# Performance work log

Measured on AMD Instinct MI355X. Metric: run time of the kernel, lower is better.

The kernel has to match this reference:

```python
import jax, jax.numpy as jnp
import numpy as np

B, L, H, NH, DH, FF, NL, REL = 2, 1024, 256, 8, 32, 1024, 2, 100
SCALE = np.sqrt(DH).astype(np.float32)
EPS = 1e-5


def _ln(x, g, b):
    m = jnp.mean(x, axis=-1, keepdims=True)
    v = jnp.mean(jnp.square(x - m), axis=-1, keepdims=True)
    return (x - m) * jax.lax.rsqrt(v + EPS) * g + b


def setup_inputs() -> dict:
    key = jax.random.key(0)
    ks = jax.random.split(key, 20)
    s = 0.02
    Ek = jax.random.normal(ks[0], (REL, DH), jnp.float32) * s
    Ev = jax.random.normal(ks[1], (REL, DH), jnp.float32) * s
    Ek = Ek.at[0].set(0.0)  # padding_idx=0
    Ev = Ev.at[0].set(0.0)
    return {
        "inputs": jax.random.normal(ks[2], (B, L, H), jnp.float32),
        "Wq": jax.random.normal(ks[3], (NL, H, H), jnp.float32) * s,
        "Wk": jax.random.normal(ks[4], (NL, H, H), jnp.float32) * s,
        "Wv": jax.random.normal(ks[5], (NL, H, H), jnp.float32) * s,
        "Wo": jax.random.normal(ks[6], (NL, H, H), jnp.float32) * s,
        "bo": jnp.zeros((NL, H), jnp.float32),
        "W1": jax.random.normal(ks[7], (NL, H, FF), jnp.float32) * s,
        "b1": jnp.zeros((NL, FF), jnp.float32),
        "W2": jax.random.normal(ks[8], (NL, FF, H), jnp.float32) * s,
        "b2": jnp.zeros((NL, H), jnp.float32),
        "ln1_g": jnp.ones((NL, H), jnp.float32),
        "ln1_b": jnp.zeros((NL, H), jnp.float32),
        "ln2_g": jnp.ones((NL, H), jnp.float32),
        "ln2_b": jnp.zeros((NL, H), jnp.float32),
        "Ek": Ek,
        "Ev": Ev,
        "relations": jax.random.randint(ks[9], (B, L, L), 0, REL, jnp.int32),
        "relations_mask": jax.random.randint(ks[10], (B, L, L), 0, 2, jnp.int32).astype(bool),
    }


def reference(inputs, Wq, Wk, Wv, Wo, bo, W1, b1, W2, b2,
              ln1_g, ln1_b, ln2_g, ln2_b, Ek, Ev, relations, relations_mask):
    # relation embeddings shared across layers and heads: (B,L,L,DH)
    rel_k = Ek[relations]
    rel_v = Ev[relations]
    neg = relations_mask.astype(jnp.float32) * (-1e20)  # (B,L,L)
    x = inputs
    for l in range(NL):
        q = (x @ Wq[l]).reshape(B, L, NH, DH)
        k = (x @ Wk[l]).reshape(B, L, NH, DH)
        v = (x @ Wv[l]).reshape(B, L, NH, DH)
        # scores: q.(k_j + rel_k[i,j]) decomposed to avoid (B,H,L,L,DH)
        e = (jnp.einsum('bihd,bjhd->bhij', q, k)
             + jnp.einsum('bihd,bijd->bhij', q, rel_k)) / SCALE
        e = e + neg[:, None, :, :]
        a = jax.nn.softmax(e, axis=-1)  # (B,NH,L,L)
        o = (jnp.einsum('bhij,bjhd->bihd', a, v)
             + jnp.einsum('bhij,bijd->bihd', a, rel_v)).reshape(B, L, H)
        o = o @ Wo[l] + bo[l]
        x = _ln(x + o, ln1_g[l], ln1_b[l])
        ff = jax.nn.relu(x @ W1[l] + b1[l]) @ W2[l] + b2[l]
        x = _ln(x + ff, ln2_g[l], ln2_b[l])
    return x
```

## Files before the change

kernel.cpp:

```cpp
#include <hip/hip_runtime.h>


typedef unsigned short ushortt;
typedef __attribute__((ext_vector_type(8))) short short8;
typedef __attribute__((ext_vector_type(4))) float f32x4;

__device__ __forceinline__ ushortt f2bf(float f) {
  union { float f; unsigned int u; } c; c.f = f;
  unsigned int r = c.u + 0x7fffu + ((c.u >> 16) & 1u);
  return (ushortt)(r >> 16);
}
__device__ __forceinline__ unsigned int pk2(float a, float b) {
  return (unsigned int)f2bf(a) | ((unsigned int)f2bf(b) << 16);
}

__global__ void wcvt_all_k(const float* __restrict__ Wq, const float* __restrict__ Wk,
                           const float* __restrict__ Wv, const float* __restrict__ Wo,
                           const float* __restrict__ W1, const float* __restrict__ W2,
                           ushortt* __restrict__ wbuf) {
  int i = blockIdx.x * blockDim.x + threadIdx.x;
  int st = gridDim.x * blockDim.x;
  for (; i < 1572864; i += st) {
    int l = (i >= 786432) ? 1 : 0;
    int e = i - (l ? 786432 : 0);
    size_t o_w = (size_t)l * 65536, o_w1 = (size_t)l * 262144;
    float v;
    if (e < 262144) {
      int which = e >> 16;
      int loc = e & 65535;
      int k = loc & 255, n = loc >> 8;
      const float* W = (which == 0) ? Wq : (which == 1) ? Wk : (which == 2) ? Wv : Wo;
      v = W[o_w + ((size_t)k << 8) + n];
    } else if (e < 524288) {
      int loc = e - 262144;
      int k = loc & 255, n = loc >> 8;
      v = W1[o_w1 + ((size_t)k << 10) + n];
    } else {
      int loc = e - 524288;
      int k = loc & 1023, n = loc >> 10;
      v = W2[o_w1 + ((size_t)k << 8) + n];
    }
    wbuf[i] = f2bf(v);
  }
}

__global__ __launch_bounds__(256) void cvt_bf_k(
    const float* __restrict__ in, ushortt* __restrict__ out, int n) {
  int idx = (blockIdx.x * 256 + threadIdx.x) * 8;
  if (idx >= n) return;
  float4 f0 = *(const float4*)(in + idx);
  float4 f1 = *(const float4*)(in + idx + 4);
  uint4 u;
  u.x = pk2(f0.x, f0.y); u.y = pk2(f0.z, f0.w);
  u.z = pk2(f1.x, f1.y); u.w = pk2(f1.z, f1.w);
  *(uint4*)(out + idx) = u;
}

__global__ __launch_bounds__(256) void relpack_k(
    const int* __restrict__ rel, const int* __restrict__ msk,
    unsigned char* __restrict__ relc2,
    const float* __restrict__ Ev, float* __restrict__ EvT) {
  int g = blockIdx.x * blockDim.x + threadIdx.x;
  const int4* r4 = (const int4*)rel;
  const int4* m4 = (const int4*)msk;
  int4 r = r4[g];
  int4 m = m4[g];
  int b = g >> 18;
  int rem = g & 262143;
  int i = rem >> 8;
  int j4 = (rem & 255) << 2;
  size_t base = ((size_t)b << 20) + ((size_t)(i >> 3) << 13) + (i & 7);
  relc2[base + ((size_t)(j4 + 0) << 3)] = (unsigned char)(m.x ? 128 : r.x);
  relc2[base + ((size_t)(j4 + 1) << 3)] = (unsigned char)(m.y ? 128 : r.y);
  relc2[base + ((size_t)(j4 + 2) << 3)] = (unsigned char)(m.z ? 128 : r.z);
  relc2[base + ((size_t)(j4 + 3) << 3)] = (unsigned char)(m.w ? 128 : r.w);
  if (g < 3200) {
    int d = g / 100, rr = g - d * 100;
    EvT[d * 100 + rr] = Ev[(rr << 5) + d];
  }
}

__device__ __forceinline__ void mgemm_body(
    const ushortt* __restrict__ A, const ushortt* __restrict__ BT,
    const float* __restrict__ bias, size_t boff,
    float* __restrict__ C, ushortt* __restrict__ cbf,
    int m0, int n0, int N, int K, int kbeg, int kend, int relu, int kvmode)
{
  __shared__ ushortt As[64 * 72];
  __shared__ ushortt Bs[64 * 72];
  int tid = threadIdx.x;
  int wv = tid >> 6, lane = tid & 63;
  int quad = lane >> 4, mr = lane & 15;
  int sm = tid >> 2, k16 = (tid & 3) << 4;

  const ushortt* ap = A + (size_t)(m0 + sm) * K + k16;
  const ushortt* bp = BT + (size_t)(n0 + sm) * K + k16;

  uint4 ra0 = *(const uint4*)(ap + kbeg);
  uint4 ra1 = *(const uint4*)(ap + kbeg + 8);
  uint4 rb0 = *(const uint4*)(bp + kbeg);
  uint4 rb1 = *(const uint4*)(bp + kbeg + 8);

  f32x4 acc[4] = {};
  for (int k0 = kbeg; k0 < kend; k0 += 64) {
    *(uint4*)(&As[sm * 72 + k16])     = ra0;
    *(uint4*)(&As[sm * 72 + k16 + 8]) = ra1;
    *(uint4*)(&Bs[sm * 72 + k16])     = rb0;
    *(uint4*)(&Bs[sm * 72 + k16 + 8]) = rb1;
    __syncthreads();
    if (k0 + 64 < kend) {
      ra0 = *(const uint4*)(ap + k0 + 64);
      ra1 = *(const uint4*)(ap + k0 + 72);
      rb0 = *(const uint4*)(bp + k0 + 64);
      rb1 = *(const uint4*)(bp + k0 + 72);
    }
#pragma unroll
    for (int kh = 0; kh < 2; ++kh) {
      short8 af = *(const short8*)(&As[(wv * 16 + mr) * 72 + (kh << 5) + quad * 8]);
#pragma unroll
      for (int nt = 0; nt < 4; ++nt) {
        short8 bf = *(const short8*)(&Bs[(nt * 16 + mr) * 72 + (kh << 5) + quad * 8]);
        acc[nt] = __builtin_amdgcn_mfma_f32_16x16x32_bf16(af, bf, acc[nt], 0, 0, 0);
      }
    }
    __syncthreads();
  }
#pragma unroll
  for (int nt = 0; nt < 4; ++nt) {
#pragma unroll
    for (int r = 0; r < 4; ++r) {
      int m = m0 + wv * 16 + quad * 4 + r;
      int n = n0 + nt * 16 + mr;
      float v = acc[nt][r];
      if (bias) v += bias[boff + n];
      if (relu) v = fmaxf(v, 0.f);
      if (kvmode == 3) {
        C[(size_t)m * N + n] = v;
        int b = m >> 10, i = m & 1023, h = n >> 5, d = n & 31;
        cbf[(size_t)(((b << 3) + h) * 1024 + i) * 32 + d] =
            f2bf(v * 0.17677669529663687f);
      } else if (kvmode == 1) {
        int b = m >> 10, i = m & 1023, h = n >> 5, d = n & 31;
        cbf[(size_t)(((b << 3) + h) * 32 + d) * 1024 + i] = f2bf(v);
      } else if (kvmode == 2) {
        int b = m >> 10, i = m & 1023, h = n >> 5, d = n & 31;
        cbf[(size_t)(((b << 3) + h) * 1024 + i) * 32 + d] = f2bf(v);
      } else if (cbf) {
        cbf[(size_t)m * N + n] = f2bf(v);
      } else {
        C[(size_t)m * N + n] = v;
      }
    }
  }
}

__global__ __launch_bounds__(256) void mgemm_k(
    const ushortt* __restrict__ A, const ushortt* __restrict__ BT,
    const float* __restrict__ bias, size_t boff,
    float* __restrict__ C0, float* __restrict__ C1, ushortt* __restrict__ cbf,
    int N, int K, int relu)
{
  int kidx = blockIdx.z;
  int kc = K / gridDim.z;
  int kbeg = kidx * kc;
  mgemm_body(A, BT, kidx ? nullptr : bias, boff,
             kidx ? C1 : C0, cbf,
             blockIdx.y * 64, blockIdx.x * 64, N, K, kbeg, kbeg + kc, relu, 0);
}

__global__ __launch_bounds__(256) void mqkv_k(
    const ushortt* __restrict__ xbf, const ushortt* __restrict__ WT,
    float* __restrict__ q, ushortt* __restrict__ qbf,
    ushortt* __restrict__ kbf, ushortt* __restrict__ vTbf)
{
  int sel = blockIdx.x >> 2;
  const ushortt* BT = WT + (size_t)sel * 65536;
  int mode = (sel == 0) ? 3 : (sel == 1) ? 2 : 1;
  mgemm_body(xbf, BT, nullptr, 0,
             (sel == 0) ? q : nullptr,
             (sel == 0) ? qbf : (sel == 1) ? kbf : vTbf,
             blockIdx.y * 64, (blockIdx.x & 3) * 64, 256, 256, 0, 256, 0, mode);
}

__global__ __launch_bounds__(256) void attn_mf8_k(
    const ushortt* __restrict__ qbf, const ushortt* __restrict__ kbf,
    const ushortt* __restrict__ vTbf, const float* __restrict__ q,
    const float* __restrict__ Ek, const float* __restrict__ EvT,
    const unsigned char* __restrict__ relc2, ushortt* __restrict__ out)
{
  __shared__ __align__(16) ushortt pbf[8 * 1028];
  __shared__ float expq[800];
  __shared__ float wbin[8 * 108];

  int tid = threadIdx.x;
  int wv = tid >> 6, lane = tid & 63;
  int quad = lane >> 4, mr = lane & 15;
  int bid = blockIdx.x;
  int tile = bid & 127;
  int h = (bid >> 7) & 7;
  int b = bid >> 10;
  int i0 = tile << 3;

  float* ekl = (float*)pbf;
  float* qs  = (float*)pbf + 3300;

  int iqsel = quad & 1;
  int iq = iqsel << 2;
  int jofs = ((quad >> 1) << 4) + mr;
  int jbase = wv << 8;
  const unsigned int* rc2 =
      (const unsigned int*)(relc2 + (((size_t)(b << 7) + tile) << 13));
  unsigned int rcw[8];
#pragma unroll
  for (int t = 0; t < 8; ++t)
    rcw[t] = rc2[(((jbase + (t << 5) + jofs)) << 1) + iqsel];

  for (int p = tid; p < 3200; p += 256)
    ekl[(p >> 5) * 33 + (p & 31)] = Ek[p];
  {
    int i = tid >> 5, d = tid & 31;
    qs[i * 33 + d] = q[(((size_t)(b * 1024 + i0 + i) * 8 + h) << 5) + d]
                     * 0.17677669529663687f;
  }
  for (int p = tid; p < 864; p += 256) wbin[p] = 0.f;

  const ushortt* qsrc = qbf + ((size_t)(b * 8 + h) << 15);
  short8 qf = *(const short8*)(qsrc + (((size_t)i0 + (mr & 7)) << 5) + quad * 8);

  const ushortt* ks = kbf + ((size_t)(b * 8 + h) << 15);
  const ushortt* vs = vTbf + ((size_t)(b * 8 + h) << 15);
  short8 kfa = *(const short8*)(ks + ((size_t)(jbase + mr) << 5) + quad * 8);
  short8 kfb = *(const short8*)(ks + ((size_t)(jbase + 16 + mr) << 5) + quad * 8);
  __syncthreads();

  for (int p = tid; p < 800; p += 256) {
    int i = p / 100, r = p - i * 100;
    float s = 0.f;
#pragma unroll
    for (int d = 0; d < 32; ++d) s += qs[i * 33 + d] * ekl[r * 33 + d];
    expq[p] = __expf(s);
  }
  __syncthreads();

#pragma unroll
  for (int t = 0; t < 8; ++t) {
    int j0 = jbase + (t << 5);
    short8 ka = kfa, kb = kfb;
    if (t < 7) {
      kfa = *(const short8*)(ks + ((size_t)(j0 + 32 + mr) << 5) + quad * 8);
      kfb = *(const short8*)(ks + ((size_t)(j0 + 48 + mr) << 5) + quad * 8);
    }
    f32x4 z = {};
    f32x4 sa = __builtin_amdgcn_mfma_f32_16x16x32_bf16(qf, ka, z, 0, 0, 0);
    f32x4 sb = __builtin_amdgcn_mfma_f32_16x16x32_bf16(qf, kb, z, 0, 0, 0);
    int j = j0 + jofs;
    unsigned int w = rcw[t];
#pragma unroll
    for (int r = 0; r < 4; ++r) {
      int i = iq + r;
      float sv = (quad >= 2) ? sb[r] : sa[r];
      unsigned int c = (w >> (r << 3)) & 255u;
      float p = 0.f;
      if (c < 128u) {
        p = __expf(sv) * expq[i * 100 + (int)c];
        atomicAdd(&wbin[i * 108 + (int)c], p);
      }
      pbf[i * 1028 + j] = f2bf(p);
    }
  }
  __syncthreads();

  float* pvpart = expq;
  float* pvtot  = expq + 256;
  int d0 = (wv & 1) << 4;
  int k0 = (wv >> 1) << 9;
  int prow = (mr & 7) * 1028;
  f32x4 acc0 = {}, acc1 = {};
  short8 vf = *(const short8*)(vs + ((size_t)(d0 + mr) << 10) + k0 + quad * 8);
#pragma unroll
  for (int kt = 0; kt < 16; ++kt) {
    int kk = k0 + (kt << 5);
    short8 vcur = vf;
    if (kt < 15)
      vf = *(const short8*)(vs + ((size_t)(d0 + mr) << 10) + k0 + ((kt + 1) << 5) + quad * 8);
    short8 pf = *(const short8*)(&pbf[prow + kk + quad * 8]);
    if (kt & 1)
      acc1 = __builtin_amdgcn_mfma_f32_16x16x32_bf16(pf, vcur, acc1, 0, 0, 0);
    else
      acc0 = __builtin_amdgcn_mfma_f32_16x16x32_bf16(pf, vcur, acc0, 0, 0, 0);
  }
  f32x4 acc;
#pragma unroll
  for (int r = 0; r < 4; ++r) acc[r] = acc0[r] + acc1[r];
  if (wv >= 2 && quad < 2) {
#pragma unroll
    for (int r = 0; r < 4; ++r)
      pvpart[((wv & 1) << 7) + (quad * 4 + r) * 16 + mr] = acc[r];
  }
  __syncthreads();
  if (wv < 2 && quad < 2) {
#pragma unroll
    for (int r = 0; r < 4; ++r) {
      int i = quad * 4 + r;
      pvtot[i * 32 + d0 + mr] = acc[r] + pvpart[((wv & 1) << 7) + i * 16 + mr];
    }
  }
  __syncthreads();

  {
    int i = tid >> 5, d = tid & 31;
    const float4* evt = (const float4*)(EvT + d * 100);
    const float4* wb4 = (const float4*)(&wbin[i * 108]);
    float e0 = 0.f, e1 = 0.f, e2 = 0.f, e3 = 0.f;
    float s0 = 0.f, s1 = 0.f, s2 = 0.f, s3 = 0.f;
#pragma unroll
    for (int rq = 0; rq < 25; ++rq) {
      float4 e4 = evt[rq];
      float4 w4 = wb4[rq];
      e0 += w4.x * e4.x; s0 += w4.x;
      e1 += w4.y * e4.y; s1 += w4.y;
      e2 += w4.z * e4.z; s2 += w4.z;
      e3 += w4.w * e4.w; s3 += w4.w;
    }
    float ev = (e0 + e1) + (e2 + e3);
    float den = (s0 + s1) + (s2 + s3);
    out[(((size_t)(b * 1024 + i0 + i) * 8 + h) << 5) + d] =
        f2bf((pvtot[i * 32 + d] + ev) / den);
  }
}

__global__ __launch_bounds__(256) void ln_k(
    const float* __restrict__ x, const float* __restrict__ o,
    const float* __restrict__ o2,
    const float* __restrict__ g, const float* __restrict__ bta, size_t eoff,
    float* __restrict__ xo, ushortt* __restrict__ xbf, float* __restrict__ fout)
{
  __shared__ float red[256];
  int row = blockIdx.x, t = threadIdx.x;
  size_t idx = (size_t)row * 256 + t;
  float r = x[idx] + o[idx];
  if (o2) r += o2[idx];
  red[t] = r;
  __syncthreads();
  for (int off = 128; off > 0; off >>= 1) {
    if (t < off) red[t] += red[t + off];
    __syncthreads();
  }
  float mean = red[0] * (1.f / 256.f);
  __syncthreads();
  float dv = r - mean;
  red[t] = dv * dv;
  __syncthreads();
  for (int off = 128; off > 0; off >>= 1) {
    if (t < off) red[t] += red[t + off];
    __syncthreads();
  }
  float var = red[0] * (1.f / 256.f);
  float val = dv * rsqrtf(var + 1e-5f) * g[eoff + t] + bta[eoff + t];
  xo[idx] = val;
  xbf[idx] = f2bf(val);
  if (fout) fout[idx] = val;
}

extern "C" void kernel_launch(void* const* d_in, const int* in_sizes, int n_in,
                              void* d_out, int out_size, void* d_ws, size_t ws_size,
                              hipStream_t stream) {
  const float* inp  = (const float*)d_in[0];
  const float* Wq   = (const float*)d_in[1];
  const float* Wk   = (const float*)d_in[2];
  const float* Wv   = (const float*)d_in[3];
  const float* Wo   = (const float*)d_in[4];
  const float* bo   = (const float*)d_in[5];
  const float* W1   = (const float*)d_in[6];
  const float* b1   = (const float*)d_in[7];
  const float* W2   = (const float*)d_in[8];
  const float* b2   = (const float*)d_in[9];
  const float* ln1g = (const float*)d_in[10];
  const float* ln1b = (const float*)d_in[11];
  const float* ln2g = (const float*)d_in[12];
  const float* ln2b = (const float*)d_in[13];
  const float* Ek   = (const float*)d_in[14];
  const float* Ev   = (const float*)d_in[15];
  const int*   rel  = (const int*)d_in[16];
  const int*   msk  = (const int*)d_in[17];

  const size_t SZ = 524288;
  float* x        = (float*)d_ws;
  float* q        = x + SZ;
  ushortt* kbf    = (ushortt*)(q + SZ);
  ushortt* vTbf   = kbf + SZ;
  ushortt* attnbf = vTbf + SZ;
  ushortt* xbf    = attnbf + SZ;
  float* tmp      = (float*)(xbf + SZ);
  ushortt* wbuf   = (ushortt*)(tmp + SZ);
  unsigned char* relc2 = (unsigned char*)(wbuf + 1572864);
  float* EvT      = (float*)(relc2 + 2097152);
  float* tmp2     = (float*)((char*)EvT + 16384);
  ushortt* inpbf  = (ushortt*)tmp2;
  ushortt* qbf    = (ushortt*)(tmp2 + SZ);
  ushortt* ffh    = (ushortt*)q;

  dim3 blk(256);
  wcvt_all_k<<<3072, blk, 0, stream>>>(Wq, Wk, Wv, Wo, W1, W2, wbuf);
  relpack_k<<<2048, blk, 0, stream>>>(rel, msk, relc2, Ev, EvT);
  cvt_bf_k<<<256, blk, 0, stream>>>(inp, inpbf, 524288);

  for (int l = 0; l < 2; ++l) {
    size_t o_b  = (size_t)l * 256;
    size_t o_b1 = (size_t)l * 1024;
    const ushortt* xinbf = (l == 0) ? inpbf : xbf;
    const float* xin = (l == 0) ? inp : x;
    ushortt* wl = wbuf + (size_t)l * 786432;

    mqkv_k<<<dim3(12, 32), blk, 0, stream>>>(xinbf, wl, q, qbf, kbf, vTbf);

    attn_mf8_k<<<2048, blk, 0, stream>>>(qbf, kbf, vTbf, q, Ek, EvT,
                                         relc2, attnbf);

    mgemm_k<<<dim3(4, 32, 2), blk, 0, stream>>>(attnbf, wl + 196608,
                                                bo, o_b, tmp, tmp2, nullptr,
                                                256, 256, 0);
    ln_k<<<2048, blk, 0, stream>>>(xin, tmp, tmp2, ln1g, ln1b, o_b, x, xbf, nullptr);

    mgemm_k<<<dim3(16, 32, 1), blk, 0, stream>>>(xbf, wl + 262144,
                                                 b1, o_b1, nullptr, nullptr, ffh,
                                                 1024, 256, 1);
    mgemm_k<<<dim3(4, 32, 2), blk, 0, stream>>>(ffh, wl + 524288,
                                                b2, o_b, tmp, tmp2, nullptr,
                                                256, 1024, 0);
    ln_k<<<2048, blk, 0, stream>>>(x, tmp, tmp2, ln2g, ln2b, o_b, x, xbf,
                                   (l == 1) ? (float*)d_out : nullptr);
  }
}
```

Before: 361.1 us.

## Process 16 query rows per attention block to fill MFMA tiles

The attention kernel now handles 16 query rows per block instead of 8, halving the grid to 1024 blocks. The 16x16 MFMA tiles were previously half wasted on duplicated rows; now every row carries real work, and each K/V fragment load is reused across twice as many queries. Relation codes are prefetched per step alongside K rather than held all at once in registers. The cost is doubled shared memory per block (larger pbf, expq and wbin) and fewer blocks, which may reduce occupancy and latency hiding.

```diff
diff --git a/kernel.cpp b/kernel.cpp
--- a/kernel.cpp
+++ b/kernel.cpp
@@ -188,52 +188,50 @@
     const float* __restrict__ Ek, const float* __restrict__ EvT,
     const unsigned char* __restrict__ relc2, ushortt* __restrict__ out)
 {
-  __shared__ __align__(16) ushortt pbf[8 * 1028];
-  __shared__ float expq[800];
-  __shared__ float wbin[8 * 108];
+  __shared__ __align__(16) ushortt pbf[16 * 1028];
+  __shared__ float expq[1600];
+  __shared__ float wbin[16 * 108];
 
   int tid = threadIdx.x;
   int wv = tid >> 6, lane = tid & 63;
   int quad = lane >> 4, mr = lane & 15;
   int bid = blockIdx.x;
-  int tile = bid & 127;
-  int h = (bid >> 7) & 7;
-  int b = bid >> 10;
-  int i0 = tile << 3;
+  int tile = bid & 63;
+  int h = (bid >> 6) & 7;
+  int b = bid >> 9;
+  int i0 = tile << 4;
 
   float* ekl = (float*)pbf;
   float* qs  = (float*)pbf + 3300;
 
-  int iqsel = quad & 1;
-  int iq = iqsel << 2;
-  int jofs = ((quad >> 1) << 4) + mr;
-  int jbase = wv << 8;
-  const unsigned int* rc2 =
-      (const unsigned int*)(relc2 + (((size_t)(b << 7) + tile) << 13));
-  unsigned int rcw[8];
-#pragma unroll
-  for (int t = 0; t < 8; ++t)
-    rcw[t] = rc2[(((jbase + (t << 5) + jofs)) << 1) + iqsel];
-
   for (int p = tid; p < 3200; p += 256)
     ekl[(p >> 5) * 33 + (p & 31)] = Ek[p];
-  {
-    int i = tid >> 5, d = tid & 31;
+#pragma unroll
+  for (int pp = 0; pp < 2; ++pp) {
+    int p = tid + (pp << 8);
+    int i = p >> 5, d = p & 31;
     qs[i * 33 + d] = q[(((size_t)(b * 1024 + i0 + i) * 8 + h) << 5) + d]
                      * 0.17677669529663687f;
   }
-  for (int p = tid; p < 864; p += 256) wbin[p] = 0.f;
+  for (int p = tid; p < 1728; p += 256) wbin[p] = 0.f;
 
   const ushortt* qsrc = qbf + ((size_t)(b * 8 + h) << 15);
-  short8 qf = *(const short8*)(qsrc + (((size_t)i0 + (mr & 7)) << 5) + quad * 8);
+  short8 qf = *(const short8*)(qsrc + (((size_t)i0 + mr) << 5) + quad * 8);
+
+  const unsigned int* rc2d = (const unsigned int*)(relc2 + ((size_t)b << 20));
+  int gsh = ((tile << 1) + (quad >> 1)) << 11;
+  int dsel = quad & 1;
 
   const ushortt* ks = kbf + ((size_t)(b * 8 + h) << 15);
   const ushortt* vs = vTbf + ((size_t)(b * 8 + h) << 15);
+  int jbase = wv << 8;
   short8 kfa = *(const short8*)(ks + ((size_t)(jbase + mr) << 5) + quad * 8);
   short8 kfb = *(const short8*)(ks + ((size_t)(jbase + 16 + mr) << 5) + quad * 8);
-  __syncthreads();
-
-  for (int p = tid; p < 800; p += 256) {
+  unsigned int rwa = rc2d[gsh + ((jbase + mr) << 1) + dsel];
+  unsigned int rwb = rc2d[gsh + ((jbase + 16 + mr) << 1) + dsel];
+  __syncthreads();
+
+  for (int p = tid; p < 1600; p += 256) {
     int i = p / 100, r = p - i * 100;
     float s = 0.f;
 #pragma unroll
@@ -246,35 +244,44 @@
   for (int t = 0; t < 8; ++t) {
     int j0 = jbase + (t << 5);
     short8 ka = kfa, kb = kfb;
+    unsigned int wa = rwa, wb = rwb;
     if (t < 7) {
       kfa = *(const short8*)(ks + ((size_t)(j0 + 32 + mr) << 5) + quad * 8);
       kfb = *(const short8*)(ks + ((size_t)(j0 + 48 + mr) << 5) + quad * 8);
+      rwa = rc2d[gsh + ((j0 + 32 + mr) << 1) + dsel];
+      rwb = rc2d[gsh + ((j0 + 48 + mr) << 1) + dsel];
     }
     f32x4 z = {};
     f32x4 sa = __builtin_amdgcn_mfma_f32_16x16x32_bf16(qf, ka, z, 0, 0, 0);
     f32x4 sb = __builtin_amdgcn_mfma_f32_16x16x32_bf16(qf, kb, z, 0, 0, 0);
-    int j = j0 + jofs;
-    unsigned int w = rcw[t];
+    int ja = j0 + mr, jb = j0 + 16 + mr;
 #pragma unroll
     for (int r = 0; r < 4; ++r) {
-      int i = iq + r;
-      float sv = (quad >= 2) ? sb[r] : sa[r];
-      unsigned int c = (w >> (r << 3)) & 255u;
-      float p = 0.f;
-      if (c < 128u) {
-        p = __expf(sv) * expq[i * 100 + (int)c];
-        atomicAdd(&wbin[i * 108 + (int)c], p);
+      int i = quad * 4 + r;
+      unsigned int ca = (wa >> (r << 3)) & 255u;
+      float pa = 0.f;
+      if (ca < 128u) {
+        pa = __expf(sa[r]) * expq[i * 100 + (int)ca];
+        atomicAdd(&wbin[i * 108 + (int)ca], pa);
       }
-      pbf[i * 1028 + j] = f2bf(p);
+      pbf[i * 1028 + ja] = f2bf(pa);
+      unsigned int cb = (wb >> (r << 3)) & 255u;
+      float pb = 0.f;
+      if (cb < 128u) {
+        pb = __expf(sb[r]) * expq[i * 100 + (int)cb];
+        atomicAdd(&wbin[i * 108 + (int)cb], pb);
+      }
+      pbf[i * 1028 + jb] = f2bf(pb);
     }
   }
   __syncthreads();
 
   float* pvpart = expq;
-  float* pvtot  = expq + 256;
-  int d0 = (wv & 1) << 4;
-  int k0 = (wv >> 1) << 9;
-  int prow = (mr & 7) * 1028;
+  int dhalf = wv & 1;
+  int d0 = dhalf << 4;
+  int kq = wv >> 1;
+  int k0 = kq << 9;
+  int prow = mr * 1028;
   f32x4 acc0 = {}, acc1 = {};
   short8 vf = *(const short8*)(vs + ((size_t)(d0 + mr) << 10) + k0 + quad * 8);
 #pragma unroll
@@ -292,23 +299,28 @@
   f32x4 acc;
 #pragma unroll
   for (int r = 0; r < 4; ++r) acc[r] = acc0[r] + acc1[r];
-  if (wv >= 2 && quad < 2) {
-#pragma unroll
-    for (int r = 0; r < 4; ++r)
-      pvpart[((wv & 1) << 7) + (quad * 4 + r) * 16 + mr] = acc[r];
-  }
-  __syncthreads();
-  if (wv < 2 && quad < 2) {
+  if (kq == 1) {
 #pragma unroll
     for (int r = 0; r < 4; ++r) {
       int i = quad * 4 + r;
-      pvtot[i * 32 + d0 + mr] = acc[r] + pvpart[((wv & 1) << 7) + i * 16 + mr];
-    }
-  }
-  __syncthreads();
-
-  {
-    int i = tid >> 5, d = tid & 31;
+      pvpart[(dhalf << 8) + i * 16 + mr] = acc[r];
+    }
+  }
+  __syncthreads();
+  float* pvtot = (float*)pbf;
+  if (kq == 0) {
+#pragma unroll
+    for (int r = 0; r < 4; ++r) {
+      int i = quad * 4 + r;
+      pvtot[i * 32 + d0 + mr] = acc[r] + pvpart[(dhalf << 8) + i * 16 + mr];
+    }
+  }
+  __syncthreads();
+
+#pragma unroll
+  for (int pp = 0; pp < 2; ++pp) {
+    int p = tid + (pp << 8);
+    int i = p >> 5, d = p & 31;
     const float4* evt = (const float4*)(EvT + d * 100);
     const float4* wb4 = (const float4*)(&wbin[i * 108]);
     float e0 = 0.f, e1 = 0.f, e2 = 0.f, e3 = 0.f;
@@ -414,7 +426,7 @@
 
     mqkv_k<<<dim3(12, 32), blk, 0, stream>>>(xinbf, wl, q, qbf, kbf, vTbf);
 
-    attn_mf8_k<<<2048, blk, 0, stream>>>(qbf, kbf, vTbf, q, Ek, EvT,
+    attn_mf8_k<<<1024, blk, 0, stream>>>(qbf, kbf, vTbf, q, Ek, EvT,
                                          relc2, attnbf);
 
     mgemm_k<<<dim3(4, 32, 2), blk, 0, stream>>>(attnbf, wl + 196608,
```

Measured after the change: 382.8 us. +6.0%, slower.
